# Kernel optimization log

Measured on AMD Instinct MI355X. Metric: run time of the kernel, lower is better.

## Reference

```python
import jax, jax.numpy as jnp
import numpy as np

B, T, D, H = 2, 2048, 1024, 16
DK = D // H

def setup_inputs() -> dict:
    key = jax.random.key(0)
    ks = jax.random.split(key, 7)
    s = 1.0 / np.sqrt(D)
    return {
        "query": jax.random.normal(ks[0], (B, T, D), jnp.float32),
        "key":   jax.random.normal(ks[1], (B, T, D), jnp.float32),
        "value": jax.random.normal(ks[2], (B, T, D), jnp.float32),
        "W_q": jax.random.normal(ks[3], (D, D), jnp.float32) * s,
        "W_k": jax.random.normal(ks[4], (D, D), jnp.float32) * s,
        "W_v": jax.random.normal(ks[5], (D, D), jnp.float32) * s,
        "W_o": jax.random.normal(ks[6], (D, D), jnp.float32) * s,
    }

def reference(query, key, value, W_q, W_k, W_v, W_o):
    # torch nn.Linear(bias=False): y = x @ W.T with W of shape [out, in]
    q = jnp.einsum('btd,ed->bte', query, W_q).reshape(B, T, H, DK).transpose(0, 2, 1, 3)
    k = jnp.einsum('btd,ed->bte', key,   W_k).reshape(B, T, H, DK).transpose(0, 2, 1, 3)
    v = jnp.einsum('btd,ed->bte', value, W_v).reshape(B, T, H, DK).transpose(0, 2, 1, 3)
    # scores: [B, H, T_q, T_k]
    scores = jnp.einsum('bhqd,bhkd->bhqk', q, k) / jnp.sqrt(jnp.float32(DK))
    weights = jax.nn.softmax(scores, axis=-1)  # dropout p=0.0 -> identity
    attn = jnp.einsum('bhqk,bhkd->bhqd', weights, v)
    attn = attn.transpose(0, 2, 1, 3).reshape(B, T, D)
    out = jnp.einsum('btd,ed->bte', attn, W_o)
    return out, weights
```

## Files before the change

### kernel.cpp

```cpp
#include <hip/hip_runtime.h>
#include <hip/hip_bf16.h>

#define B_  2
#define T_  2048
#define D_  1024
#define H_  16
#define DK_ 64
#define M_  (B_*T_)

typedef unsigned short u16;
typedef short s8v  __attribute__((ext_vector_type(8)));
typedef short s4v  __attribute__((ext_vector_type(4)));
typedef float f4v  __attribute__((ext_vector_type(4)));

__device__ inline u16 f2bf(float f) {
    union { float f; unsigned u; } v; v.f = f;
    unsigned u = v.u;
    u += 0x7fffu + ((u >> 16) & 1u);
    return (u16)(u >> 16);
}

__global__ __launch_bounds__(256) void cvtA(
    const float* __restrict__ s0, const float* __restrict__ s1, const float* __restrict__ s2,
    u16* __restrict__ dst)
{
    const int seg = blockIdx.y;
    const float* s = (seg == 0) ? s0 : (seg == 1) ? s1 : s2;
    u16* d = dst + (size_t)seg * 4194304;
    size_t i = (size_t)blockIdx.x * 256 + threadIdx.x;
    float4 v = ((const float4*)s)[i];
    ushort4 o;
    o.x = f2bf(v.x); o.y = f2bf(v.y); o.z = f2bf(v.z); o.w = f2bf(v.w);
    ((ushort4*)d)[i] = o;
}

__global__ __launch_bounds__(256) void cvtB(
    const float* __restrict__ s0, const float* __restrict__ s1,
    const float* __restrict__ s2, const float* __restrict__ s3,
    u16* __restrict__ dst)
{
    const int seg = blockIdx.y;
    const float* s = (seg == 0) ? s0 : (seg == 1) ? s1 : (seg == 2) ? s2 : s3;
    u16* d = dst + (size_t)seg * 1048576;
    size_t i = (size_t)blockIdx.x * 256 + threadIdx.x;
    float4 v = ((const float4*)s)[i];
    ushort4 o;
    o.x = f2bf(v.x); o.y = f2bf(v.y); o.z = f2bf(v.z); o.w = f2bf(v.w);
    ((ushort4*)d)[i] = o;
}

__global__ __launch_bounds__(256) void proj_qkv(
    const u16* __restrict__ Xq, const u16* __restrict__ Xk, const u16* __restrict__ Xv,
    const u16* __restrict__ Wq, const u16* __restrict__ Wk, const u16* __restrict__ Wv,
    u16* __restrict__ Qb, u16* __restrict__ Kb, u16* __restrict__ Vb)
{
    int z = blockIdx.z;
    const u16* X = (z == 0) ? Xq : (z == 1) ? Xk : Xv;
    const u16* W = (z == 0) ? Wq : (z == 1) ? Wk : Wv;
    u16*       Y = (z == 0) ? Qb : (z == 1) ? Kb : Vb;

    const int lane = threadIdx.x & 63;
    const int wave = threadIdx.x >> 6;
    const int c    = lane & 15;
    const int quad = lane >> 4;

    const int m0 = blockIdx.y * 64 + wave * 16;
    const int n0 = blockIdx.x * 64;

    const u16* arow  = X + (size_t)(m0 + c) * D_ + quad * 8;
    const u16* brow0 = W + (size_t)(n0 + c) * D_ + quad * 8;

    __shared__ __attribute__((aligned(16))) u16 vt[64][76];

    f4v acc[4] = {};
    for (int k0 = 0; k0 < D_; k0 += 32) {
        s8v a = *(const s8v*)(arow + k0);
#pragma unroll
        for (int j = 0; j < 4; ++j) {
            s8v b = *(const s8v*)(brow0 + (size_t)j * 16 * D_ + k0);
            acc[j] = __builtin_amdgcn_mfma_f32_16x16x32_bf16(a, b, acc[j], 0, 0, 0);
        }
    }
    if (z != 2) {
#pragma unroll
        for (int j = 0; j < 4; ++j) {
#pragma unroll
            for (int r = 0; r < 4; ++r) {
                int m = m0 + quad * 4 + r;
                int e = n0 + j * 16 + c;
                int bb = m >> 11, t = m & (T_ - 1);
                int h = e >> 6,  d = e & 63;
                Y[((size_t)(bb * H_ + h) * T_ + t) * DK_ + d] = f2bf(acc[j][r]);
            }
        }
    } else {
#pragma unroll
        for (int j = 0; j < 4; ++j)
#pragma unroll
            for (int r = 0; r < 4; ++r)
                vt[wave * 16 + quad * 4 + r][j * 16 + c] = f2bf(acc[j][r]);
        __syncthreads();
        const int hh  = n0 >> 6;
        const int mb  = blockIdx.y * 64;
        const int bb2 = mb >> 11;
        const int t0  = mb & (T_ - 1);
        const int d   = lane;
        u16 tmp[16];
#pragma unroll
        for (int i = 0; i < 16; ++i) tmp[i] = vt[wave * 16 + i][d];
        s8v v0, v1;
#pragma unroll
        for (int j = 0; j < 8; ++j) { v0[j] = (short)tmp[j]; v1[j] = (short)tmp[8 + j]; }
        u16* dst = Y + ((size_t)(bb2 * H_ + hh) * DK_ + d) * T_ + t0 + wave * 16;
        *(s8v*)dst       = v0;
        *(s8v*)(dst + 8) = v1;
    }
}

__global__ __launch_bounds__(256) void attn_kernel(
    const u16* __restrict__ Qb, const u16* __restrict__ Kb, const u16* __restrict__ VbT,
    float* __restrict__ weights, u16* __restrict__ ctx)
{
    const int lid  = blockIdx.x;
    const int bh   = lid & 31;
    const int q0   = (lid >> 5) * 16;
    const int lane = threadIdx.x & 63;
    const int wave = threadIdx.x >> 6;
    const int c    = lane & 15;
    const int quad = lane >> 4;

    const u16* Qh = Qb  + (size_t)bh * T_ * DK_;
    const u16* Kh = Kb  + (size_t)bh * T_ * DK_;
    const u16* Vt = VbT + (size_t)bh * DK_ * T_;

    __shared__ __attribute__((aligned(16))) char pool[4 * 16 * 68 * 4];
    __shared__ float wl[4][16];
    __shared__ float rowInvS[16];
    u16   (*pw)[16][76]  = (u16   (*)[16][76])pool;
    float (*red)[16][68] = (float (*)[16][68])pool;

    const u16* qrow = Qh + (size_t)(q0 + c) * DK_ + quad * 8;
    s8v aq0 = *(const s8v*)(qrow);
    s8v aq1 = *(const s8v*)(qrow + 32);

    float lp[4] = {0.f, 0.f, 0.f, 0.f};
    for (int kt = wave; kt < T_ / 16; kt += 4) {
        const u16* krow = Kh + (size_t)(kt * 16 + c) * DK_ + quad * 8;
        s8v b0 = *(const s8v*)(krow);
        s8v b1 = *(const s8v*)(krow + 32);
        f4v s = {};
        s = __builtin_amdgcn_mfma_f32_16x16x32_bf16(aq0, b0, s, 0, 0, 0);
        s = __builtin_amdgcn_mfma_f32_16x16x32_bf16(aq1, b1, s, 0, 0, 0);
#pragma unroll
        for (int r = 0; r < 4; ++r) lp[r] += __expf(s[r] * 0.125f);
    }
#pragma unroll
    for (int r = 0; r < 4; ++r) {
        float v = lp[r];
        v += __shfl_xor(v, 1); v += __shfl_xor(v, 2);
        v += __shfl_xor(v, 4); v += __shfl_xor(v, 8);
        if (c == 0) wl[wave][quad * 4 + r] = v;
    }
    __syncthreads();
    if (threadIdx.x < 16)
        rowInvS[threadIdx.x] = 1.0f / (wl[0][threadIdx.x] + wl[1][threadIdx.x] +
                                       wl[2][threadIdx.x] + wl[3][threadIdx.x]);
    __syncthreads();
    float riv[4];
#pragma unroll
    for (int r = 0; r < 4; ++r) riv[r] = rowInvS[quad * 4 + r];

    f4v acc[4] = {};
    for (int c64 = wave; c64 < T_ / 64; c64 += 4) {
        const int key0 = c64 * 64;
#pragma unroll
        for (int tt = 0; tt < 4; ++tt) {
            const u16* krow = Kh + (size_t)(key0 + tt * 16 + c) * DK_ + quad * 8;
            s8v b0 = *(const s8v*)(krow);
            s8v b1 = *(const s8v*)(krow + 32);
            f4v s = {};
            s = __builtin_amdgcn_mfma_f32_16x16x32_bf16(aq0, b0, s, 0, 0, 0);
            s = __builtin_amdgcn_mfma_f32_16x16x32_bf16(aq1, b1, s, 0, 0, 0);
            float* wrow = weights + ((size_t)bh * T_ + q0) * T_ + key0 + tt * 16 + c;
#pragma unroll
            for (int r = 0; r < 4; ++r) {
                float p = __expf(s[r] * 0.125f) * riv[r];
                pw[wave][quad * 4 + r][tt * 16 + c] = f2bf(p);
                __builtin_nontemporal_store(p, wrow + (size_t)(quad * 4 + r) * T_);
            }
        }
#pragma unroll
        for (int kk = 0; kk < 64; kk += 32) {
            const u16* prow = &pw[wave][c][kk + quad * 8];
            s4v alo = *(const s4v*)(prow);
            s4v ahi = *(const s4v*)(prow + 4);
            s8v af;
#pragma unroll
            for (int j = 0; j < 4; ++j) { af[j] = alo[j]; af[4 + j] = ahi[j]; }
#pragma unroll
            for (int n = 0; n < 4; ++n) {
                s8v bv = *(const s8v*)(Vt + (size_t)(n * 16 + c) * T_ + key0 + kk + quad * 8);
                acc[n] = __builtin_amdgcn_mfma_f32_16x16x32_bf16(af, bv, acc[n], 0, 0, 0);
            }
        }
    }

    __syncthreads();
#pragma unroll
    for (int n = 0; n < 4; ++n)
#pragma unroll
        for (int r = 0; r < 4; ++r)
            red[wave][quad * 4 + r][n * 16 + c] = acc[n][r];
    __syncthreads();

    const int bb = bh >> 4, h = bh & 15;
    for (int e = threadIdx.x; e < 16 * 64; e += 256) {
        int row = e >> 6, d = e & 63;
        float v = red[0][row][d] + red[1][row][d] + red[2][row][d] + red[3][row][d];
        ctx[((size_t)(bb * T_ + q0 + row)) * D_ + h * 64 + d] = f2bf(v);
    }
}

__global__ __launch_bounds__(256) void out_proj(
    const u16* __restrict__ X, const u16* __restrict__ W, float* __restrict__ Y)
{
    const int lane = threadIdx.x & 63;
    const int wave = threadIdx.x >> 6;
    const int c    = lane & 15;
    const int quad = lane >> 4;

    const int m0 = blockIdx.y * 64 + wave * 16;
    const int n0 = blockIdx.x * 64;

    const u16* arow  = X + (size_t)(m0 + c) * D_ + quad * 8;
    const u16* brow0 = W + (size_t)(n0 + c) * D_ + quad * 8;

    f4v acc[4] = {};
    for (int k0 = 0; k0 < D_; k0 += 32) {
        s8v a = *(const s8v*)(arow + k0);
#pragma unroll
        for (int j = 0; j < 4; ++j) {
            s8v b = *(const s8v*)(brow0 + (size_t)j * 16 * D_ + k0);
            acc[j] = __builtin_amdgcn_mfma_f32_16x16x32_bf16(a, b, acc[j], 0, 0, 0);
        }
    }
#pragma unroll
    for (int j = 0; j < 4; ++j) {
#pragma unroll
        for (int r = 0; r < 4; ++r) {
            int m = m0 + quad * 4 + r;
            int e = n0 + j * 16 + c;
            Y[(size_t)m * D_ + e] = acc[j][r];
        }
    }
}

extern "C" void kernel_launch(void* const* d_in, const int* in_sizes, int n_in,
                              void* d_out, int out_size, void* d_ws, size_t ws_size,
                              hipStream_t stream) {
    const float* query = (const float*)d_in[0];
    const float* key_  = (const float*)d_in[1];
    const float* value = (const float*)d_in[2];
    const float* W_q   = (const float*)d_in[3];
    const float* W_k   = (const float*)d_in[4];
    const float* W_v   = (const float*)d_in[5];
    const float* W_o   = (const float*)d_in[6];

    float* out_attn = (float*)d_out;
    float* weights  = (float*)d_out + (size_t)B_ * T_ * D_;

    const size_t perX = (size_t)M_ * D_;
    const size_t perW = (size_t)D_ * D_;
    u16* Xb  = (u16*)d_ws;
    u16* Wb  = Xb + 3 * perX;
    u16* Qb  = Wb + 4 * perW;
    u16* Kb  = Qb + perX;
    u16* Vb  = Kb + perX;
    u16* ctx = Vb + perX;

    dim3 gA(4096, 3, 1);
    cvtA<<<gA, 256, 0, stream>>>(query, key_, value, Xb);
    dim3 gB(1024, 4, 1);
    cvtB<<<gB, 256, 0, stream>>>(W_q, W_k, W_v, W_o, Wb);

    dim3 gproj(D_ / 64, M_ / 64, 3);
    proj_qkv<<<gproj, 256, 0, stream>>>(Xb, Xb + perX, Xb + 2 * perX,
                                        Wb, Wb + perW, Wb + 2 * perW,
                                        Qb, Kb, Vb);

    attn_kernel<<<dim3((T_ / 16) * B_ * H_, 1, 1), 256, 0, stream>>>(Qb, Kb, Vb, weights, ctx);

    dim3 gout(D_ / 64, M_ / 64, 1);
    out_proj<<<gout, 256, 0, stream>>>(ctx, Wb + 3 * perW, out_attn);
}
```

Measured before the change: 1.138 ms.

## Prefetch K/V into registers and coalesce attention-weight stores via LDS staging

The attention kernel's first pass now double-buffers K tile loads in registers so memory latency overlaps the MFMA/exp work. The second pass preloads K and V fragments per 64-key chunk and stages the fp32 probabilities in LDS. From there it writes full 64-wide rows of the weights matrix with coalesced nontemporal stores, instead of scattered 16-wide stores. bf16 conversion uses packed v_cvt_pk_bf16_f32. Launch bounds request 3 blocks per CU, and the projection GEMM loops get unroll 2, trading extra register pressure for more memory-level parallelism.

```diff
diff --git a/kernel.cpp b/kernel.cpp
--- a/kernel.cpp
+++ b/kernel.cpp
@@ -10,7 +10,6 @@
 
 typedef unsigned short u16;
 typedef short s8v  __attribute__((ext_vector_type(8)));
-typedef short s4v  __attribute__((ext_vector_type(4)));
 typedef float f4v  __attribute__((ext_vector_type(4)));
 
 __device__ inline u16 f2bf(float f) {
@@ -73,6 +72,7 @@
     __shared__ __attribute__((aligned(16))) u16 vt[64][76];
 
     f4v acc[4] = {};
+#pragma unroll 2
     for (int k0 = 0; k0 < D_; k0 += 32) {
         s8v a = *(const s8v*)(arow + k0);
 #pragma unroll
@@ -117,7 +117,25 @@
     }
 }
 
-__global__ __launch_bounds__(256) void attn_kernel(
+#define LOADK(c64, dst) do {                                                   \
+    const u16* kb_ = Kh + ((size_t)((c64) * 64) + c) * DK_ + quad * 8;         \
+    _Pragma("unroll")                                                          \
+    for (int tt_ = 0; tt_ < 4; ++tt_) {                                        \
+        dst[2*tt_]   = *(const s8v*)(kb_ + (size_t)tt_ * 16 * DK_);            \
+        dst[2*tt_+1] = *(const s8v*)(kb_ + (size_t)tt_ * 16 * DK_ + 32);       \
+    } } while (0)
+
+#define ACCUM(kf) do {                                                         \
+    _Pragma("unroll")                                                          \
+    for (int tt_ = 0; tt_ < 4; ++tt_) {                                        \
+        f4v s_ = {};                                                           \
+        s_ = __builtin_amdgcn_mfma_f32_16x16x32_bf16(aq0, kf[2*tt_],   s_, 0, 0, 0); \
+        s_ = __builtin_amdgcn_mfma_f32_16x16x32_bf16(aq1, kf[2*tt_+1], s_, 0, 0, 0); \
+        _Pragma("unroll")                                                      \
+        for (int r_ = 0; r_ < 4; ++r_) lp[r_] += __expf(s_[r_] * 0.125f);      \
+    } } while (0)
+
+__global__ __launch_bounds__(256, 3) void attn_kernel(
     const u16* __restrict__ Qb, const u16* __restrict__ Kb, const u16* __restrict__ VbT,
     float* __restrict__ weights, u16* __restrict__ ctx)
 {
@@ -133,26 +151,25 @@
     const u16* Kh = Kb  + (size_t)bh * T_ * DK_;
     const u16* Vt = VbT + (size_t)bh * DK_ * T_;
 
-    __shared__ __attribute__((aligned(16))) char pool[4 * 16 * 68 * 4];
+    __shared__ __attribute__((aligned(16))) float pool[4][16][68];
     __shared__ float wl[4][16];
     __shared__ float rowInvS[16];
-    u16   (*pw)[16][76]  = (u16   (*)[16][76])pool;
-    float (*red)[16][68] = (float (*)[16][68])pool;
 
     const u16* qrow = Qh + (size_t)(q0 + c) * DK_ + quad * 8;
     s8v aq0 = *(const s8v*)(qrow);
     s8v aq1 = *(const s8v*)(qrow + 32);
 
     float lp[4] = {0.f, 0.f, 0.f, 0.f};
-    for (int kt = wave; kt < T_ / 16; kt += 4) {
-        const u16* krow = Kh + (size_t)(kt * 16 + c) * DK_ + quad * 8;
-        s8v b0 = *(const s8v*)(krow);
-        s8v b1 = *(const s8v*)(krow + 32);
-        f4v s = {};
-        s = __builtin_amdgcn_mfma_f32_16x16x32_bf16(aq0, b0, s, 0, 0, 0);
-        s = __builtin_amdgcn_mfma_f32_16x16x32_bf16(aq1, b1, s, 0, 0, 0);
-#pragma unroll
-        for (int r = 0; r < 4; ++r) lp[r] += __expf(s[r] * 0.125f);
+    {
+        s8v kA[8], kB[8];
+        LOADK(wave, kA);
+#pragma unroll
+        for (int i = 0; i < 8; i += 2) {
+            LOADK(wave + 4 * (i + 1), kB);
+            ACCUM(kA);
+            if (i + 2 < 8) LOADK(wave + 4 * (i + 2), kA);
+            ACCUM(kB);
+        }
     }
 #pragma unroll
     for (int r = 0; r < 4; ++r) {
@@ -171,37 +188,50 @@
     for (int r = 0; r < 4; ++r) riv[r] = rowInvS[quad * 4 + r];
 
     f4v acc[4] = {};
+    float* pf = &pool[wave][0][0];
     for (int c64 = wave; c64 < T_ / 64; c64 += 4) {
         const int key0 = c64 * 64;
+        s8v kf[8], vf[8];
+        LOADK(c64, kf);
+#pragma unroll
+        for (int kk2 = 0; kk2 < 2; ++kk2)
+#pragma unroll
+            for (int n = 0; n < 4; ++n)
+                vf[kk2 * 4 + n] = *(const s8v*)(Vt + (size_t)(n * 16 + c) * T_ +
+                                                key0 + kk2 * 32 + quad * 8);
 #pragma unroll
         for (int tt = 0; tt < 4; ++tt) {
-            const u16* krow = Kh + (size_t)(key0 + tt * 16 + c) * DK_ + quad * 8;
-            s8v b0 = *(const s8v*)(krow);
-            s8v b1 = *(const s8v*)(krow + 32);
-            f4v s = {};
-            s = __builtin_amdgcn_mfma_f32_16x16x32_bf16(aq0, b0, s, 0, 0, 0);
-            s = __builtin_amdgcn_mfma_f32_16x16x32_bf16(aq1, b1, s, 0, 0, 0);
-            float* wrow = weights + ((size_t)bh * T_ + q0) * T_ + key0 + tt * 16 + c;
+            f4v s_ = {};
+            s_ = __builtin_amdgcn_mfma_f32_16x16x32_bf16(aq0, kf[2*tt],   s_, 0, 0, 0);
+            s_ = __builtin_amdgcn_mfma_f32_16x16x32_bf16(aq1, kf[2*tt+1], s_, 0, 0, 0);
 #pragma unroll
             for (int r = 0; r < 4; ++r) {
-                float p = __expf(s[r] * 0.125f) * riv[r];
-                pw[wave][quad * 4 + r][tt * 16 + c] = f2bf(p);
-                __builtin_nontemporal_store(p, wrow + (size_t)(quad * 4 + r) * T_);
+                float p = __expf(s_[r] * 0.125f) * riv[r];
+                pf[(quad * 4 + r) * 68 + tt * 16 + c] = p;
             }
         }
 #pragma unroll
-        for (int kk = 0; kk < 64; kk += 32) {
-            const u16* prow = &pw[wave][c][kk + quad * 8];
-            s4v alo = *(const s4v*)(prow);
-            s4v ahi = *(const s4v*)(prow + 4);
-            s8v af;
-#pragma unroll
-            for (int j = 0; j < 4; ++j) { af[j] = alo[j]; af[4 + j] = ahi[j]; }
-#pragma unroll
-            for (int n = 0; n < 4; ++n) {
-                s8v bv = *(const s8v*)(Vt + (size_t)(n * 16 + c) * T_ + key0 + kk + quad * 8);
-                acc[n] = __builtin_amdgcn_mfma_f32_16x16x32_bf16(af, bv, acc[n], 0, 0, 0);
-            }
+        for (int kk2 = 0; kk2 < 2; ++kk2) {
+            const float* pr = &pf[c * 68 + kk2 * 32 + quad * 8];
+            f4v plo = *(const f4v*)(pr);
+            f4v phi = *(const f4v*)(pr + 4);
+            unsigned w0, w1, w2, w3;
+            asm("v_cvt_pk_bf16_f32 %0, %1, %2" : "=v"(w0) : "v"(plo[0]), "v"(plo[1]));
+            asm("v_cvt_pk_bf16_f32 %0, %1, %2" : "=v"(w1) : "v"(plo[2]), "v"(plo[3]));
+            asm("v_cvt_pk_bf16_f32 %0, %1, %2" : "=v"(w2) : "v"(phi[0]), "v"(phi[1]));
+            asm("v_cvt_pk_bf16_f32 %0, %1, %2" : "=v"(w3) : "v"(phi[2]), "v"(phi[3]));
+            union { unsigned u[4]; s8v v8; } pu;
+            pu.u[0] = w0; pu.u[1] = w1; pu.u[2] = w2; pu.u[3] = w3;
+#pragma unroll
+            for (int n = 0; n < 4; ++n)
+                acc[n] = __builtin_amdgcn_mfma_f32_16x16x32_bf16(pu.v8, vf[kk2 * 4 + n],
+                                                                 acc[n], 0, 0, 0);
+        }
+        float* wbase = weights + ((size_t)bh * T_ + q0) * T_ + key0;
+#pragma unroll
+        for (int row = 0; row < 16; ++row) {
+            float pv = pf[row * 68 + lane];
+            __builtin_nontemporal_store(pv, wbase + (size_t)row * T_ + lane);
         }
     }
 
@@ -210,13 +240,13 @@
     for (int n = 0; n < 4; ++n)
 #pragma unroll
         for (int r = 0; r < 4; ++r)
-            red[wave][quad * 4 + r][n * 16 + c] = acc[n][r];
+            pool[wave][quad * 4 + r][n * 16 + c] = acc[n][r];
     __syncthreads();
 
     const int bb = bh >> 4, h = bh & 15;
     for (int e = threadIdx.x; e < 16 * 64; e += 256) {
         int row = e >> 6, d = e & 63;
-        float v = red[0][row][d] + red[1][row][d] + red[2][row][d] + red[3][row][d];
+        float v = pool[0][row][d] + pool[1][row][d] + pool[2][row][d] + pool[3][row][d];
         ctx[((size_t)(bb * T_ + q0 + row)) * D_ + h * 64 + d] = f2bf(v);
     }
 }
@@ -236,6 +266,7 @@
     const u16* brow0 = W + (size_t)(n0 + c) * D_ + quad * 8;
 
     f4v acc[4] = {};
+#pragma unroll 2
     for (int k0 = 0; k0 < D_; k0 += 32) {
         s8v a = *(const s8v*)(arow + k0);
 #pragma unroll
```

Measured after the change: 1.140 ms. Within noise of the previous version (+0.2%).
